# Kernel optimization log

Hardware: AMD Instinct MI355X
Metric: run time of the kernel (lower is better)

## Reference

```python
import jax, jax.numpy as jnp
import numpy as np

B, T, D, H = 2, 2048, 1024, 4
DK, DV = 1024, 2048          # key_dim = d_model*expand_k, value_dim = d_model*expand_v
HK, HV = DK // H, DV // H    # 256, 512 per-head dims
LR = 16                      # gate_low_rank_dim
EPS = 1e-5
GATE_NORM = 16.0             # gate_logit_normalizer


def _xavier(k, shape, gain):
    fan_in, fan_out = shape
    lim = gain * np.sqrt(6.0 / (fan_in + fan_out))
    return jax.random.uniform(k, shape, jnp.float32, -lim, lim)


def setup_inputs() -> dict:
    key = jax.random.key(0)
    ks = jax.random.split(key, 10)
    g_qkv = 2 ** (-2.5)
    return {
        "x": jax.random.normal(ks[0], (B, T, D), jnp.float32),
        "Wq": _xavier(ks[1], (D, DK), g_qkv),
        "Wk": _xavier(ks[2], (D, DK), g_qkv),
        "Wv": _xavier(ks[3], (D, DV), g_qkv),
        "Wg": _xavier(ks[4], (D, DV), g_qkv),
        "gk_w1": _xavier(ks[5], (D, LR), g_qkv),
        "gk_w2": _xavier(ks[6], (LR, DK), g_qkv),
        "gk_b": jnp.zeros((DK,), jnp.float32),
        "Wo": _xavier(ks[7], (DV, D), 2 ** (-1)),
        "rms_w": jnp.ones((HV,), jnp.float32),
    }


def _gla_scan(q, k, v, g):
    # q,k,g: [T, hk]; v: [T, hv]. Recurrence S_t = diag(exp(g_t)) S_{t-1} + k_t v_t^T; o_t = q_t @ S_t
    S0 = jnp.zeros((q.shape[-1], v.shape[-1]), q.dtype)

    def step(S, inp):
        qt, kt, vt, gt = inp
        S = jnp.exp(gt)[:, None] * S + kt[:, None] * vt[None, :]
        return S, qt @ S

    return jax.lax.scan(step, S0, (q, k, v, g))[1]  # [T, hv]


def _forward(x, Wq, Wk, Wv, Wg, gk_w1, gk_w2, gk_b, Wo, rms_w):
    b, t = x.shape[0], x.shape[1]
    scale = HK ** -0.5
    # projections -> [b, h, t, d_head]
    q = (x @ Wq).reshape(b, t, H, HK).transpose(0, 2, 1, 3) * scale
    k = (x @ Wk).reshape(b, t, H, HK).transpose(0, 2, 1, 3)
    v = (x @ Wv).reshape(b, t, H, HV).transpose(0, 2, 1, 3)
    # low-rank forget gate, log-space, fp32
    gl = (x @ gk_w1) @ gk_w2 + gk_b
    g = (jax.nn.log_sigmoid(gl.astype(jnp.float32)) / GATE_NORM)
    g = g.reshape(b, t, H, HK).transpose(0, 2, 1, 3)
    # per-(batch, head) linear-attention recurrence
    o = jax.vmap(jax.vmap(_gla_scan))(q, k, v, g)  # [b, h, t, hv]
    # group RMSNorm over head_v_dim
    o = o.transpose(0, 2, 1, 3)  # [b, t, h, hv]
    o = o * jax.lax.rsqrt(jnp.mean(o * o, axis=-1, keepdims=True) + EPS) * rms_w
    # output gate (swish) + out projection
    o = o.reshape(b, t, DV) * jax.nn.silu(x @ Wg)
    return o @ Wo  # [b, t, d_model]


def reference(x, Wq, Wk, Wv, Wg, gk_w1, gk_w2, gk_b, Wo, rms_w):
    return _forward(x, Wq, Wk, Wv, Wg, gk_w1, gk_w2, gk_b, Wo, rms_w)
```

## Files before the change

### kernel.cpp

```cpp
#include <hip/hip_runtime.h>
#include <cstdint>
#include <cstddef>


typedef unsigned short u16;
typedef __attribute__((ext_vector_type(8))) short s8v;
typedef __attribute__((ext_vector_type(4))) float f4v;

__device__ __forceinline__ u16 f2b(float f) {
  unsigned u = __builtin_bit_cast(unsigned, f);
  unsigned r = u + 0x7FFFu + ((u >> 16) & 1u);
  return (u16)(r >> 16);
}
__device__ __forceinline__ float b2f(u16 h) {
  unsigned u = ((unsigned)h) << 16;
  return __builtin_bit_cast(float, u);
}

__device__ __forceinline__ void cp16(const void* g, void* l) {
  __builtin_amdgcn_global_load_lds(
      (const __attribute__((address_space(1))) unsigned int*)g,
      (__attribute__((address_space(3))) unsigned int*)l, 16, 0, 0);
}

__device__ __forceinline__ void stage_tile(const u16* g, int ld, u16* lds,
                                           int wv, int ln) {
  const int q = (ln & 3) ^ ((ln >> 3) & 3);
#pragma unroll
  for (int i = 0; i < 2; ++i) {
    const int c = wv * 2 + i;
    const u16* src = g + (size_t)(c * 16 + (ln >> 2)) * ld + q * 8;
    cp16(src, lds + c * 512);
  }
}

__device__ __forceinline__ void gemm_core(
    const u16* __restrict__ A, int lda, const u16* __restrict__ BT, int ldb,
    int K, u16* As, u16* Bs, f4v acc[4][4])
{
  const int tid = threadIdx.x;
  const int ln = tid & 63, wv = tid >> 6;
  const int arow = (wv >> 1) * 64 + (ln & 15);
  const int brow = (wv & 1) * 64 + (ln & 15);
  const int koff = (((ln >> 4) ^ ((ln >> 1) & 3)) * 8);
  const int nt = K >> 5;
  stage_tile(A, lda, As, wv, ln);
  stage_tile(BT, ldb, Bs, wv, ln);
  stage_tile(A + 32, lda, As + 4096, wv, ln);
  stage_tile(BT + 32, ldb, Bs + 4096, wv, ln);
  stage_tile(A + 64, lda, As + 8192, wv, ln);
  stage_tile(BT + 64, ldb, Bs + 8192, wv, ln);
  int slot = 0;
  for (int t = 0; t < nt; ++t) {
    const int rem = nt - 1 - t;
    if (rem >= 2)      asm volatile("s_waitcnt vmcnt(8)" ::: "memory");
    else if (rem == 1) asm volatile("s_waitcnt vmcnt(4)" ::: "memory");
    else               asm volatile("s_waitcnt vmcnt(0)" ::: "memory");
    __builtin_amdgcn_s_barrier();
    __builtin_amdgcn_sched_barrier(0);
    const u16* Ab = As + slot * 4096;
    const u16* Bb = Bs + slot * 4096;
    s8v af[4], bf[4];
#pragma unroll
    for (int f = 0; f < 4; ++f)
      af[f] = *(const s8v*)(Ab + (arow + f * 16) * 32 + koff);
#pragma unroll
    for (int f = 0; f < 4; ++f)
      bf[f] = *(const s8v*)(Bb + (brow + f * 16) * 32 + koff);
#pragma unroll
    for (int mf = 0; mf < 4; ++mf)
#pragma unroll
      for (int nf = 0; nf < 4; ++nf)
        acc[mf][nf] = __builtin_amdgcn_mfma_f32_16x16x32_bf16(
            af[mf], bf[nf], acc[mf][nf], 0, 0, 0);
    __builtin_amdgcn_sched_barrier(0);
    __builtin_amdgcn_s_barrier();
    if (t + 3 < nt) {
      stage_tile(A + (t + 3) * 32, lda, As + slot * 4096, wv, ln);
      stage_tile(BT + (t + 3) * 32, ldb, Bs + slot * 4096, wv, ln);
    }
    slot = (slot == 2) ? 0 : slot + 1;
  }
}

#define EPI_SETUP                                            \
  const int tid = threadIdx.x;                               \
  const int ln = tid & 63, wv = tid >> 6;                    \
  const int wr = wv >> 1, wc = wv & 1;

#define ZERO_ACC(acc)                                        \
  _Pragma("unroll")                                          \
  for (int zi = 0; zi < 4; ++zi)                             \
    _Pragma("unroll")                                        \
    for (int zj = 0; zj < 4; ++zj)                           \
      acc[zi][zj] = (f4v){0.f, 0.f, 0.f, 0.f};

__global__ __launch_bounds__(256) void cast_b(const float* __restrict__ in,
                                              u16* __restrict__ out) {
  const int i = blockIdx.x * 256 + threadIdx.x;
  const float4 v = ((const float4*)in)[i];
  u16* p = out + i * 4;
  p[0] = f2b(v.x); p[1] = f2b(v.y); p[2] = f2b(v.z); p[3] = f2b(v.w);
}

__global__ __launch_bounds__(256) void wtrans_all(
    const float* __restrict__ Wq, const float* __restrict__ Wk,
    const float* __restrict__ Wv, const float* __restrict__ Wg,
    const float* __restrict__ Wo, u16* __restrict__ WTa, u16* __restrict__ WoT)
{
  __shared__ float t[32][33];
  const int id = blockIdx.x;
  const float* src; u16* dst; int R, C, local;
  if (id < 1024)      { src = Wq; dst = WTa;           R = 1024; C = 1024; local = id; }
  else if (id < 2048) { src = Wk; dst = WTa + 1048576; R = 1024; C = 1024; local = id - 1024; }
  else if (id < 4096) { src = Wv; dst = WTa + 2097152; R = 1024; C = 2048; local = id - 2048; }
  else if (id < 6144) { src = Wg; dst = WTa + 4194304; R = 1024; C = 2048; local = id - 4096; }
  else                { src = Wo; dst = WoT;           R = 2048; C = 1024; local = id - 6144; }
  const int nx = C >> 5;
  const int c0 = (local % nx) * 32, r0 = (local / nx) * 32;
  const int lx = threadIdx.x & 31, ly = threadIdx.x >> 5;
#pragma unroll
  for (int i = 0; i < 32; i += 8)
    t[ly + i][lx] = src[(size_t)(r0 + ly + i) * C + c0 + lx];
  __syncthreads();
#pragma unroll
  for (int i = 0; i < 32; i += 8)
    dst[(size_t)(c0 + ly + i) * R + r0 + lx] = f2b(t[lx][ly + i]);
}

__global__ __launch_bounds__(256) void trans_all(
    const u16* __restrict__ kt, u16* __restrict__ ktT,
    const u16* __restrict__ vr, u16* __restrict__ vT)
{
  __shared__ u16 t[32][33];
  const int id = blockIdx.x;
  const u16* in; u16* out; int R = 2048, C, z, local;
  if (id < 4096) { in = kt; out = ktT; C = 256;  z = id >> 9;  local = id & 511; }
  else { const int i2 = id - 4096; in = vr; out = vT; C = 512; z = i2 >> 10; local = i2 & 1023; }
  const int nx = C >> 5;
  const int c0 = (local % nx) * 32, r0 = (local / nx) * 32;
  const size_t boff = (size_t)z * R * C;
  const int lx = threadIdx.x & 31, ly = threadIdx.x >> 5;
#pragma unroll
  for (int i = 0; i < 32; i += 8)
    t[ly + i][lx] = in[boff + (size_t)(r0 + ly + i) * C + c0 + lx];
  __syncthreads();
#pragma unroll
  for (int i = 0; i < 32; i += 8)
    out[boff + (size_t)(c0 + ly + i) * R + r0 + lx] = t[lx][ly + i];
}

__global__ __launch_bounds__(256) void lowrank1(
    const float* __restrict__ x, const float* __restrict__ w1,
    float* __restrict__ tmp)
{
  const int idx = blockIdx.x * 256 + threadIdx.x;
  const int m = idx >> 4, i = idx & 15;
  const float* xr = x + (size_t)m * 1024;
  float acc = 0.f;
#pragma unroll 4
  for (int kk = 0; kk < 1024; kk += 4) {
    const float4 xv = *(const float4*)(xr + kk);
    acc = fmaf(xv.x, w1[(kk + 0) * 16 + i], acc);
    acc = fmaf(xv.y, w1[(kk + 1) * 16 + i], acc);
    acc = fmaf(xv.z, w1[(kk + 2) * 16 + i], acc);
    acc = fmaf(xv.w, w1[(kk + 3) * 16 + i], acc);
  }
  tmp[idx] = acc;
}

__global__ __launch_bounds__(256) void gate_cum(
    const float* __restrict__ tmp, const float* __restrict__ w2,
    const float* __restrict__ bias, u16* __restrict__ dq, u16* __restrict__ dk,
    float* __restrict__ Dc)
{
  __shared__ float ls_t[2048];
  const int b = blockIdx.y >> 4, c = blockIdx.y & 15;
  const int h = blockIdx.x;
  const int i = threadIdx.x;
  const int n = h * 256 + i;
  const int bh = b * 4 + h;
  const float* tp = tmp + ((size_t)(b * 2048 + c * 128)) * 16;
#pragma unroll
  for (int r = 0; r < 8; ++r) ls_t[r * 256 + threadIdx.x] = tp[r * 256 + threadIdx.x];
  __syncthreads();
  float w2c[16];
#pragma unroll
  for (int r = 0; r < 16; ++r) w2c[r] = w2[r * 1024 + n];
  const float bn = bias[n];
  const size_t base = ((size_t)bh * 2048 + c * 128) * 256 + i;
  float B = 0.f;
  for (int t = 0; t < 128; ++t) {
    float gl = bn;
    const float* tr = ls_t + t * 16;
#pragma unroll
    for (int r = 0; r < 16; ++r) gl = fmaf(tr[r], w2c[r], gl);
    const float ls = fminf(gl, 0.f) - log1pf(expf(-fabsf(gl)));
    B += ls * 0.0625f;
    const float eB = expf(B);
    dq[base + (size_t)t * 256] = f2b(eB);
    dk[base + (size_t)t * 256] = f2b(1.f / eB);
  }
  Dc[(bh * 16 + c) * 256 + i] = expf(B);
}

__global__ __launch_bounds__(256) void proj_all(
    const u16* __restrict__ xb, const u16* __restrict__ WT,
    const u16* __restrict__ dq, const u16* __restrict__ dk,
    u16* __restrict__ qt, u16* __restrict__ kt,
    u16* __restrict__ vr, u16* __restrict__ gpre)
{
  __shared__ __align__(16) u16 As[12288], Bs[12288];
  const int id = blockIdx.x;
  const int xcd = id & 7, j = id >> 3;
  const int m0 = (j / 6) * 128;
  const int n0 = (xcd * 6 + (j % 6)) * 128;
  f4v acc[4][4];
  ZERO_ACC(acc)
  gemm_core(xb + (size_t)m0 * 1024, 1024, WT + (size_t)n0 * 1024, 1024, 1024,
            As, Bs, acc);
  EPI_SETUP
#pragma unroll
  for (int mf = 0; mf < 4; ++mf)
#pragma unroll
    for (int nf = 0; nf < 4; ++nf)
#pragma unroll
      for (int r = 0; r < 4; ++r) {
        const int m = m0 + wr * 64 + mf * 16 + ((ln >> 4) << 2) + r;
        const int n = n0 + wc * 64 + nf * 16 + (ln & 15);
        const float val = acc[mf][nf][r];
        const int b = m >> 11, t = m & 2047;
        if (n0 < 1024) {
          const int bh = b * 4 + (n >> 8), i = n & 255;
          const size_t off = ((size_t)bh * 2048 + t) * 256 + i;
          qt[off] = f2b(val * 0.0625f * b2f(dq[off]));
        } else if (n0 < 2048) {
          const int nn = n - 1024;
          const int bh = b * 4 + (nn >> 8), i = nn & 255;
          const size_t off = ((size_t)bh * 2048 + t) * 256 + i;
          kt[off] = f2b(val * b2f(dk[off]));
        } else if (n0 < 4096) {
          const int nn = n - 2048;
          const int bh = b * 4 + (nn >> 9), jj = nn & 511;
          vr[((size_t)bh * 2048 + t) * 512 + jj] = f2b(val);
        } else {
          gpre[(size_t)m * 2048 + (n - 4096)] = f2b(val);
        }
      }
}

__global__ __launch_bounds__(256) void scan_gemms(
    const u16* __restrict__ vT, const u16* __restrict__ ktT,
    const u16* __restrict__ qt, const u16* __restrict__ kt,
    u16* __restrict__ UT, u16* __restrict__ Aw)
{
  __shared__ __align__(16) u16 As[12288], Bs[12288];
  const int bhc = blockIdx.y, bh = bhc >> 4, c = bhc & 15;
  f4v acc[4][4];
  ZERO_ACC(acc)
  if (blockIdx.x < 8) {
    const int mt = blockIdx.x >> 1, nt = blockIdx.x & 1;
    gemm_core(vT + ((size_t)bh * 512 + mt * 128) * 2048 + c * 128, 2048,
              ktT + ((size_t)bh * 256 + nt * 128) * 2048 + c * 128, 2048, 128,
              As, Bs, acc);
    EPI_SETUP
#pragma unroll
    for (int mf = 0; mf < 4; ++mf)
#pragma unroll
      for (int nf = 0; nf < 4; ++nf)
#pragma unroll
        for (int r = 0; r < 4; ++r) {
          const int j = mt * 128 + wr * 64 + mf * 16 + ((ln >> 4) << 2) + r;
          const int i = nt * 128 + wc * 64 + nf * 16 + (ln & 15);
          UT[(((size_t)(bh * 512 + j)) * 16 + c) * 256 + i] = f2b(acc[mf][nf][r]);
        }
  } else {
    const size_t base = ((size_t)bh * 2048 + c * 128) * 256;
    gemm_core(qt + base, 256, kt + base, 256, 256, As, Bs, acc);
    EPI_SETUP
    u16* Ap = Aw + (size_t)bhc * 16384;
#pragma unroll
    for (int mf = 0; mf < 4; ++mf)
#pragma unroll
      for (int nf = 0; nf < 4; ++nf)
#pragma unroll
        for (int r = 0; r < 4; ++r) {
          const int t = wr * 64 + mf * 16 + ((ln >> 4) << 2) + r;
          const int s = wc * 64 + nf * 16 + (ln & 15);
          Ap[t * 128 + s] = (s <= t) ? f2b(acc[mf][nf][r]) : (u16)0;
        }
  }
}

__global__ __launch_bounds__(256) void state_scan(
    u16* __restrict__ UT, const float* __restrict__ Dc)
{
  const int blk = blockIdx.x;
  const int bh = blk >> 9, j = blk & 511;
  const int i = threadIdx.x;
  u16* Up = UT + ((size_t)(bh * 512 + j)) * 16 * 256 + i;
  const float* Dp = Dc + bh * 16 * 256 + i;
  float S = 0.f;
  for (int c = 0; c < 16; ++c) {
    const float u = b2f(Up[c * 256]);
    Up[c * 256] = f2b(S);
    S = Dp[c * 256] * (S + u);
  }
}

__global__ __launch_bounds__(256) void intra_k(
    const u16* __restrict__ Aw, const u16* __restrict__ qt,
    const u16* __restrict__ vT, const u16* __restrict__ UT, u16* __restrict__ ob)
{
  __shared__ __align__(16) u16 As[12288], Bs[12288];
  const int jt = blockIdx.x;
  const int bhc = blockIdx.y, bh = bhc >> 4, c = bhc & 15;
  f4v acc[4][4];
  ZERO_ACC(acc)
  gemm_core(Aw + (size_t)bhc * 16384, 128,
            vT + ((size_t)bh * 512 + jt * 128) * 2048 + c * 128, 2048, 128,
            As, Bs, acc);
  gemm_core(qt + ((size_t)bh * 2048 + c * 128) * 256, 256,
            UT + ((size_t)(bh * 512 + jt * 128)) * 4096 + (size_t)c * 256, 4096, 256,
            As, Bs, acc);
  EPI_SETUP
  const int b = bh >> 2, h = bh & 3;
#pragma unroll
  for (int mf = 0; mf < 4; ++mf)
#pragma unroll
    for (int nf = 0; nf < 4; ++nf)
#pragma unroll
      for (int r = 0; r < 4; ++r) {
        const int t = c * 128 + wr * 64 + mf * 16 + ((ln >> 4) << 2) + r;
        const int j = jt * 128 + wc * 64 + nf * 16 + (ln & 15);
        ob[((size_t)(b * 2048 + t)) * 2048 + h * 512 + j] = f2b(acc[mf][nf][r]);
      }
}

__global__ __launch_bounds__(256) void rms_silu(
    u16* __restrict__ o, const u16* __restrict__ gpre, const float* __restrict__ w)
{
  const int grp = blockIdx.x * 4 + (threadIdx.x >> 6);
  const int lane = threadIdx.x & 63;
  const size_t base = (size_t)(grp >> 2) * 2048 + (grp & 3) * 512;
  float xv[8];
  float ss = 0.f;
#pragma unroll
  for (int i = 0; i < 8; ++i) {
    xv[i] = b2f(o[base + i * 64 + lane]);
    ss = fmaf(xv[i], xv[i], ss);
  }
#pragma unroll
  for (int off = 1; off < 64; off <<= 1) ss += __shfl_xor(ss, off, 64);
  const float r = rsqrtf(ss * (1.f / 512.f) + 1e-5f);
#pragma unroll
  for (int i = 0; i < 8; ++i) {
    const int cidx = i * 64 + lane;
    const float gp = b2f(gpre[base + cidx]);
    const float sig = 1.f / (1.f + expf(-gp));
    o[base + cidx] = f2b(xv[i] * r * w[cidx] * gp * sig);
  }
}

__global__ __launch_bounds__(256) void gemm_out(
    const u16* __restrict__ ob, const u16* __restrict__ WoT,
    float* __restrict__ pout)
{
  __shared__ __align__(16) u16 As[12288], Bs[12288];
  const int id = blockIdx.x;
  const int wg = (id & 7) * 64 + (id >> 3);
  const int ks = wg >> 8;
  const int tt = wg & 255;
  const int m0 = (tt & 31) * 128, n0 = (tt >> 5) * 128;
  f4v acc[4][4];
  ZERO_ACC(acc)
  gemm_core(ob + (size_t)m0 * 2048 + ks * 1024, 2048,
            WoT + (size_t)n0 * 2048 + ks * 1024, 2048, 1024, As, Bs, acc);
  EPI_SETUP
  float* po = pout + (size_t)ks * 4194304;
#pragma unroll
  for (int mf = 0; mf < 4; ++mf)
#pragma unroll
    for (int nf = 0; nf < 4; ++nf)
#pragma unroll
      for (int r = 0; r < 4; ++r) {
        const int m = m0 + wr * 64 + mf * 16 + ((ln >> 4) << 2) + r;
        const int n = n0 + wc * 64 + nf * 16 + (ln & 15);
        po[(size_t)m * 1024 + n] = acc[mf][nf][r];
      }
}

__global__ __launch_bounds__(256) void reduce_out(
    const float* __restrict__ p, float* __restrict__ out)
{
  const int i = blockIdx.x * 256 + threadIdx.x;
  const float4 a = ((const float4*)p)[i];
  const float4 b = ((const float4*)(p + 4194304))[i];
  ((float4*)out)[i] = make_float4(a.x + b.x, a.y + b.y, a.z + b.z, a.w + b.w);
}

extern "C" void kernel_launch(void* const* d_in, const int* in_sizes, int n_in,
                              void* d_out, int out_size, void* d_ws, size_t ws_size,
                              hipStream_t stream) {
  const float* x    = (const float*)d_in[0];
  const float* Wq   = (const float*)d_in[1];
  const float* Wk   = (const float*)d_in[2];
  const float* Wv   = (const float*)d_in[3];
  const float* Wg   = (const float*)d_in[4];
  const float* w1   = (const float*)d_in[5];
  const float* w2   = (const float*)d_in[6];
  const float* gb   = (const float*)d_in[7];
  const float* Wo   = (const float*)d_in[8];
  const float* rmsw = (const float*)d_in[9];
  float* out = (float*)d_out;

  char* W = (char*)d_ws;
  u16*   xb   = (u16*)W;   W += (size_t)8  << 20;
  u16*   WTa  = (u16*)W;   W += (size_t)12 << 20;
  u16*   WoT  = (u16*)W;   W += (size_t)4  << 20;
  u16*   qt   = (u16*)W;   W += (size_t)8  << 20;
  u16*   kt   = (u16*)W;   W += (size_t)8  << 20;
  u16*   vr   = (u16*)W;   W += (size_t)16 << 20;
  u16*   vT   = (u16*)W;   W += (size_t)16 << 20;
  u16*   ktT  = (u16*)W;   W += (size_t)8  << 20;
  u16*   gpre = (u16*)W;   W += (size_t)16 << 20;
  float* tmp  = (float*)W; W += (size_t)256 << 10;
  float* Dc   = (float*)W; W += (size_t)128 << 10;
  u16*   dq   = (u16*)W;   W += (size_t)8  << 20;
  u16*   dk   = (u16*)W;   W += (size_t)8  << 20;
  u16*   UT   = (u16*)W;   W += (size_t)32 << 20;
  u16*   Aw   = (u16*)W;   W += (size_t)4  << 20;
  u16*   ob   = (u16*)W;   W += (size_t)16 << 20;
  float* pout = (float*)W; W += (size_t)32 << 20;

  hipLaunchKernelGGL(lowrank1, dim3(256), dim3(256), 0, stream, x, w1, tmp);
  hipLaunchKernelGGL(gate_cum, dim3(4, 32), dim3(256), 0, stream,
                     tmp, w2, gb, dq, dk, Dc);

  hipLaunchKernelGGL(cast_b, dim3(4096), dim3(256), 0, stream, x, xb);
  hipLaunchKernelGGL(wtrans_all, dim3(8192), dim3(256), 0, stream,
                     Wq, Wk, Wv, Wg, Wo, WTa, WoT);

  hipLaunchKernelGGL(proj_all, dim3(1536), dim3(256), 0, stream,
                     xb, WTa, dq, dk, qt, kt, vr, gpre);

  hipLaunchKernelGGL(trans_all, dim3(12288), dim3(256), 0, stream,
                     kt, ktT, vr, vT);

  hipLaunchKernelGGL(scan_gemms, dim3(9, 128), dim3(256), 0, stream,
                     vT, ktT, qt, kt, UT, Aw);
  hipLaunchKernelGGL(state_scan, dim3(4096), dim3(256), 0, stream, UT, Dc);
  hipLaunchKernelGGL(intra_k, dim3(4, 128), dim3(256), 0, stream, Aw, qt, vT, UT, ob);

  hipLaunchKernelGGL(rms_silu, dim3(4096), dim3(256), 0, stream, ob, gpre, rmsw);
  hipLaunchKernelGGL(gemm_out, dim3(512), dim3(256), 0, stream, ob, WoT, pout);
  hipLaunchKernelGGL(reduce_out, dim3(4096), dim3(256), 0, stream, pout, out);
}
```

Baseline: 307.6 us.

## Stage GEMM epilogues through LDS for vectorized stores; shrink pipeline to double buffer

GEMM epilogues in proj_all, scan_gemms and intra_k now write accumulator fragments to LDS as bf16, then read back 8-element rows so each thread issues 16-byte global stores (and 16-byte dq/dk loads) instead of scattered 2-byte writes. To fit the padded staging area in LDS, the gemm_core pipeline drops from triple to double buffering with adjusted waitcnt and prefetch distance. Coalesced writes should cut store transactions, but the shallower prefetch may expose more load latency in the main loops, and the extra LDS round trip and barrier add work to each epilogue.

```diff
diff --git a/kernel.cpp b/kernel.cpp
--- a/kernel.cpp
+++ b/kernel.cpp
@@ -48,14 +48,10 @@
   stage_tile(BT, ldb, Bs, wv, ln);
   stage_tile(A + 32, lda, As + 4096, wv, ln);
   stage_tile(BT + 32, ldb, Bs + 4096, wv, ln);
-  stage_tile(A + 64, lda, As + 8192, wv, ln);
-  stage_tile(BT + 64, ldb, Bs + 8192, wv, ln);
   int slot = 0;
   for (int t = 0; t < nt; ++t) {
-    const int rem = nt - 1 - t;
-    if (rem >= 2)      asm volatile("s_waitcnt vmcnt(8)" ::: "memory");
-    else if (rem == 1) asm volatile("s_waitcnt vmcnt(4)" ::: "memory");
-    else               asm volatile("s_waitcnt vmcnt(0)" ::: "memory");
+    if (t + 1 < nt) asm volatile("s_waitcnt vmcnt(4)" ::: "memory");
+    else            asm volatile("s_waitcnt vmcnt(0)" ::: "memory");
     __builtin_amdgcn_s_barrier();
     __builtin_amdgcn_sched_barrier(0);
     const u16* Ab = As + slot * 4096;
@@ -75,25 +71,41 @@
             af[mf], bf[nf], acc[mf][nf], 0, 0, 0);
     __builtin_amdgcn_sched_barrier(0);
     __builtin_amdgcn_s_barrier();
-    if (t + 3 < nt) {
-      stage_tile(A + (t + 3) * 32, lda, As + slot * 4096, wv, ln);
-      stage_tile(BT + (t + 3) * 32, ldb, Bs + slot * 4096, wv, ln);
+    if (t + 2 < nt) {
+      stage_tile(A + (t + 2) * 32, lda, As + slot * 4096, wv, ln);
+      stage_tile(BT + (t + 2) * 32, ldb, Bs + slot * 4096, wv, ln);
     }
-    slot = (slot == 2) ? 0 : slot + 1;
-  }
-}
-
-#define EPI_SETUP                                            \
-  const int tid = threadIdx.x;                               \
-  const int ln = tid & 63, wv = tid >> 6;                    \
-  const int wr = wv >> 1, wc = wv & 1;
-
-#define ZERO_ACC(acc)                                        \
-  _Pragma("unroll")                                          \
-  for (int zi = 0; zi < 4; ++zi)                             \
-    _Pragma("unroll")                                        \
-    for (int zj = 0; zj < 4; ++zj)                           \
-      acc[zi][zj] = (f4v){0.f, 0.f, 0.f, 0.f};
+    slot ^= 1;
+  }
+}
+
+__device__ __forceinline__ void frag_to_lds(u16* S, const f4v acc[4][4],
+                                            int ln, int wv) {
+  u16* q = S + wv * 4608;
+#pragma unroll
+  for (int mf = 0; mf < 4; ++mf)
+#pragma unroll
+    for (int nf = 0; nf < 4; ++nf)
+#pragma unroll
+      for (int r = 0; r < 4; ++r)
+        q[(mf * 16 + ((ln >> 4) << 2) + r) * 72 + nf * 16 + (ln & 15)] =
+            f2b(acc[mf][nf][r]);
+}
+
+template <typename F>
+__device__ __forceinline__ void epi_loop(u16* S, const f4v acc[4][4], F f) {
+  const int tid = threadIdx.x;
+  frag_to_lds(S, acc, tid & 63, tid >> 6);
+  __syncthreads();
+#pragma unroll
+  for (int p = 0; p < 8; ++p) {
+    const int r = p * 16 + (tid >> 4);
+    const int c0 = (tid & 15) * 8;
+    const int quad = ((r >> 6) << 1) + (c0 >> 6);
+    s8v vv = *(const s8v*)(S + quad * 4608 + (r & 63) * 72 + (c0 & 63));
+    f(r, c0, vv);
+  }
+}
 
 __global__ __launch_bounds__(256) void cast_b(const float* __restrict__ in,
                                               u16* __restrict__ out) {
@@ -210,43 +222,54 @@
     u16* __restrict__ qt, u16* __restrict__ kt,
     u16* __restrict__ vr, u16* __restrict__ gpre)
 {
-  __shared__ __align__(16) u16 As[12288], Bs[12288];
+  __shared__ __align__(16) u16 S[18432];
+  u16* As = S; u16* Bs = S + 8192;
   const int id = blockIdx.x;
-  const int xcd = id & 7, j = id >> 3;
-  const int m0 = (j / 6) * 128;
-  const int n0 = (xcd * 6 + (j % 6)) * 128;
+  const int xcd = id & 7, jb = id >> 3;
+  const int m0 = (jb / 6) * 128;
+  const int n0 = (xcd * 6 + (jb % 6)) * 128;
   f4v acc[4][4];
-  ZERO_ACC(acc)
+#pragma unroll
+  for (int zi = 0; zi < 4; ++zi)
+#pragma unroll
+    for (int zj = 0; zj < 4; ++zj) acc[zi][zj] = (f4v){0.f, 0.f, 0.f, 0.f};
   gemm_core(xb + (size_t)m0 * 1024, 1024, WT + (size_t)n0 * 1024, 1024, 1024,
             As, Bs, acc);
-  EPI_SETUP
-#pragma unroll
-  for (int mf = 0; mf < 4; ++mf)
-#pragma unroll
-    for (int nf = 0; nf < 4; ++nf)
-#pragma unroll
-      for (int r = 0; r < 4; ++r) {
-        const int m = m0 + wr * 64 + mf * 16 + ((ln >> 4) << 2) + r;
-        const int n = n0 + wc * 64 + nf * 16 + (ln & 15);
-        const float val = acc[mf][nf][r];
-        const int b = m >> 11, t = m & 2047;
-        if (n0 < 1024) {
-          const int bh = b * 4 + (n >> 8), i = n & 255;
-          const size_t off = ((size_t)bh * 2048 + t) * 256 + i;
-          qt[off] = f2b(val * 0.0625f * b2f(dq[off]));
-        } else if (n0 < 2048) {
-          const int nn = n - 1024;
-          const int bh = b * 4 + (nn >> 8), i = nn & 255;
-          const size_t off = ((size_t)bh * 2048 + t) * 256 + i;
-          kt[off] = f2b(val * b2f(dk[off]));
-        } else if (n0 < 4096) {
-          const int nn = n - 2048;
-          const int bh = b * 4 + (nn >> 9), jj = nn & 511;
-          vr[((size_t)bh * 2048 + t) * 512 + jj] = f2b(val);
-        } else {
-          gpre[(size_t)m * 2048 + (n - 4096)] = f2b(val);
-        }
-      }
+  epi_loop(S, acc, [&](int r, int c0, s8v vv) {
+    const int m = m0 + r;
+    const int n = n0 + c0;
+    const int bb = m >> 11;
+    const int t = m & 2047;
+    if (n0 < 1024) {
+      const int bh = bb * 4 + (n >> 8);
+      const int i = n & 255;
+      const size_t off = ((size_t)bh * 2048 + t) * 256 + i;
+      const s8v dv = *(const s8v*)(dq + off);
+      s8v o8;
+#pragma unroll
+      for (int e = 0; e < 8; ++e)
+        o8[e] = (short)f2b(b2f((u16)vv[e]) * 0.0625f * b2f((u16)dv[e]));
+      *(s8v*)(qt + off) = o8;
+    } else if (n0 < 2048) {
+      const int nn = n - 1024;
+      const int bh = bb * 4 + (nn >> 8);
+      const int i = nn & 255;
+      const size_t off = ((size_t)bh * 2048 + t) * 256 + i;
+      const s8v dv = *(const s8v*)(dk + off);
+      s8v o8;
+#pragma unroll
+      for (int e = 0; e < 8; ++e)
+        o8[e] = (short)f2b(b2f((u16)vv[e]) * b2f((u16)dv[e]));
+      *(s8v*)(kt + off) = o8;
+    } else if (n0 < 4096) {
+      const int nn = n - 2048;
+      const int bh = bb * 4 + (nn >> 9);
+      const int jj = nn & 511;
+      *(s8v*)(vr + ((size_t)bh * 2048 + t) * 512 + jj) = vv;
+    } else {
+      *(s8v*)(gpre + (size_t)m * 2048 + (n - 4096)) = vv;
+    }
+  });
 }
 
 __global__ __launch_bounds__(256) void scan_gemms(
@@ -254,41 +277,35 @@
     const u16* __restrict__ qt, const u16* __restrict__ kt,
     u16* __restrict__ UT, u16* __restrict__ Aw)
 {
-  __shared__ __align__(16) u16 As[12288], Bs[12288];
+  __shared__ __align__(16) u16 S[18432];
+  u16* As = S; u16* Bs = S + 8192;
   const int bhc = blockIdx.y, bh = bhc >> 4, c = bhc & 15;
   f4v acc[4][4];
-  ZERO_ACC(acc)
+#pragma unroll
+  for (int zi = 0; zi < 4; ++zi)
+#pragma unroll
+    for (int zj = 0; zj < 4; ++zj) acc[zi][zj] = (f4v){0.f, 0.f, 0.f, 0.f};
   if (blockIdx.x < 8) {
     const int mt = blockIdx.x >> 1, nt = blockIdx.x & 1;
     gemm_core(vT + ((size_t)bh * 512 + mt * 128) * 2048 + c * 128, 2048,
               ktT + ((size_t)bh * 256 + nt * 128) * 2048 + c * 128, 2048, 128,
               As, Bs, acc);
-    EPI_SETUP
-#pragma unroll
-    for (int mf = 0; mf < 4; ++mf)
-#pragma unroll
-      for (int nf = 0; nf < 4; ++nf)
-#pragma unroll
-        for (int r = 0; r < 4; ++r) {
-          const int j = mt * 128 + wr * 64 + mf * 16 + ((ln >> 4) << 2) + r;
-          const int i = nt * 128 + wc * 64 + nf * 16 + (ln & 15);
-          UT[(((size_t)(bh * 512 + j)) * 16 + c) * 256 + i] = f2b(acc[mf][nf][r]);
-        }
+    epi_loop(S, acc, [&](int r, int c0, s8v vv) {
+      const int j = mt * 128 + r;
+      const int i = nt * 128 + c0;
+      *(s8v*)(UT + (((size_t)(bh * 512 + j)) * 16 + c) * 256 + i) = vv;
+    });
   } else {
     const size_t base = ((size_t)bh * 2048 + c * 128) * 256;
     gemm_core(qt + base, 256, kt + base, 256, 256, As, Bs, acc);
-    EPI_SETUP
     u16* Ap = Aw + (size_t)bhc * 16384;
-#pragma unroll
-    for (int mf = 0; mf < 4; ++mf)
-#pragma unroll
-      for (int nf = 0; nf < 4; ++nf)
-#pragma unroll
-        for (int r = 0; r < 4; ++r) {
-          const int t = wr * 64 + mf * 16 + ((ln >> 4) << 2) + r;
-          const int s = wc * 64 + nf * 16 + (ln & 15);
-          Ap[t * 128 + s] = (s <= t) ? f2b(acc[mf][nf][r]) : (u16)0;
-        }
+    epi_loop(S, acc, [&](int r, int c0, s8v vv) {
+      s8v o8;
+#pragma unroll
+      for (int e = 0; e < 8; ++e)
+        o8[e] = (c0 + e <= r) ? vv[e] : (short)0;
+      *(s8v*)(Ap + r * 128 + c0) = o8;
+    });
   }
 }
 
@@ -300,11 +317,11 @@
   const int i = threadIdx.x;
   u16* Up = UT + ((size_t)(bh * 512 + j)) * 16 * 256 + i;
   const float* Dp = Dc + bh * 16 * 256 + i;
-  float S = 0.f;
+  float Sa = 0.f;
   for (int c = 0; c < 16; ++c) {
     const float u = b2f(Up[c * 256]);
-    Up[c * 256] = f2b(S);
-    S = Dp[c * 256] * (S + u);
+    Up[c * 256] = f2b(Sa);
+    Sa = Dp[c * 256] * (Sa + u);
   }
 }
 
@@ -312,29 +329,27 @@
     const u16* __restrict__ Aw, const u16* __restrict__ qt,
     const u16* __restrict__ vT, const u16* __restrict__ UT, u16* __restrict__ ob)
 {
-  __shared__ __align__(16) u16 As[12288], Bs[12288];
+  __shared__ __align__(16) u16 S[18432];
+  u16* As = S; u16* Bs = S + 8192;
   const int jt = blockIdx.x;
   const int bhc = blockIdx.y, bh = bhc >> 4, c = bhc & 15;
   f4v acc[4][4];
-  ZERO_ACC(acc)
+#pragma unroll
+  for (int zi = 0; zi < 4; ++zi)
+#pragma unroll
+    for (int zj = 0; zj < 4; ++zj) acc[zi][zj] = (f4v){0.f, 0.f, 0.f, 0.f};
   gemm_core(Aw + (size_t)bhc * 16384, 128,
             vT + ((size_t)bh * 512 + jt * 128) * 2048 + c * 128, 2048, 128,
             As, Bs, acc);
   gemm_core(qt + ((size_t)bh * 2048 + c * 128) * 256, 256,
             UT + ((size_t)(bh * 512 + jt * 128)) * 4096 + (size_t)c * 256, 4096, 256,
             As, Bs, acc);
-  EPI_SETUP
   const int b = bh >> 2, h = bh & 3;
-#pragma unroll
-  for (int mf = 0; mf < 4; ++mf)
-#pragma unroll
-    for (int nf = 0; nf < 4; ++nf)
-#pragma unroll
-      for (int r = 0; r < 4; ++r) {
-        const int t = c * 128 + wr * 64 + mf * 16 + ((ln >> 4) << 2) + r;
-        const int j = jt * 128 + wc * 64 + nf * 16 + (ln & 15);
-        ob[((size_t)(b * 2048 + t)) * 2048 + h * 512 + j] = f2b(acc[mf][nf][r]);
-      }
+  epi_loop(S, acc, [&](int r, int c0, s8v vv) {
+    const int t = c * 128 + r;
+    const int j = jt * 128 + c0;
+    *(s8v*)(ob + ((size_t)(b * 2048 + t)) * 2048 + h * 512 + j) = vv;
+  });
 }
 
 __global__ __launch_bounds__(256) void rms_silu(
@@ -366,17 +381,23 @@
     const u16* __restrict__ ob, const u16* __restrict__ WoT,
     float* __restrict__ pout)
 {
-  __shared__ __align__(16) u16 As[12288], Bs[12288];
+  __shared__ __align__(16) u16 S[18432];
+  u16* As = S; u16* Bs = S + 8192;
   const int id = blockIdx.x;
   const int wg = (id & 7) * 64 + (id >> 3);
   const int ks = wg >> 8;
   const int tt = wg & 255;
   const int m0 = (tt & 31) * 128, n0 = (tt >> 5) * 128;
   f4v acc[4][4];
-  ZERO_ACC(acc)
+#pragma unroll
+  for (int zi = 0; zi < 4; ++zi)
+#pragma unroll
+    for (int zj = 0; zj < 4; ++zj) acc[zi][zj] = (f4v){0.f, 0.f, 0.f, 0.f};
   gemm_core(ob + (size_t)m0 * 2048 + ks * 1024, 2048,
             WoT + (size_t)n0 * 2048 + ks * 1024, 2048, 1024, As, Bs, acc);
-  EPI_SETUP
+  const int tid = threadIdx.x;
+  const int ln = tid & 63, wv = tid >> 6;
+  const int wr = wv >> 1, wc = wv & 1;
   float* po = pout + (size_t)ks * 4194304;
 #pragma unroll
   for (int mf = 0; mf < 4; ++mf)
```

After: 277.4 us. -9.8%, faster.
